# Kernel optimization log

Measured on AMD Instinct MI355X. Metric: run time of the kernel, lower is better.

## Reference

```python
import jax, jax.numpy as jnp
import numpy as np

N = 50000
E = 600000
DIN = 128
HID = 128
NG = 64


def _gat(x, src, dst, W, a_s, a_d, b, heads, dout, concat):
    # PyG GATConv (eval mode): per-head linear, edge attention logits,
    # segment softmax over destination nodes, weighted scatter-sum.
    n = x.shape[0]
    xp = (x @ W.T).reshape(n, heads, dout)                     # [n, H, D]
    e = jax.nn.leaky_relu(jnp.sum(xp * a_s, -1)[src] + jnp.sum(xp * a_d, -1)[dst], 0.2)  # [Etot, H]
    m = jax.ops.segment_max(e, dst, num_segments=n)
    ex = jnp.exp(e - m[dst])
    alpha = ex / jax.ops.segment_sum(ex, dst, num_segments=n)[dst]
    out = jax.ops.segment_sum(xp[src] * alpha[:, :, None], dst, num_segments=n)  # [n, H, D]
    out = out.reshape(n, heads * dout) if concat else out.mean(axis=1)
    return out + b


def _forward(x, edge_index, batch, Wi1, bi1, Wi2, bi2, Wg0, As0, Ad0, bg0, Wg1, As1, Ad1, bg1, Wg2, As2, Ad2, bg2, Wg3, As3, Ad3, bg3, We1, be1, We2, be2, Wc1, bc1, Wc2, bc2, Wc3, bc3):
    n = x.shape[0]
    loops = jnp.arange(n, dtype=edge_index.dtype)              # add_self_loops=True
    src = jnp.concatenate([edge_index[0], loops])
    dst = jnp.concatenate([edge_index[1], loops])
    # input_proj (dropout is a no-op in eval)
    h = jax.nn.relu(x @ Wi1.T + bi1) @ Wi2.T + bi2
    specs = [(Wg0, As0, Ad0, bg0, 8, 16, True),
             (Wg1, As1, Ad1, bg1, 8, 16, True),
             (Wg2, As2, Ad2, bg2, 8, 16, True),
             (Wg3, As3, Ad3, bg3, 1, 128, False)]
    for i, (W, a_s, a_d, b, hd, do, cc) in enumerate(specs):
        res = h
        h = jax.nn.elu(_gat(h, src, dst, W, a_s, a_d, b, hd, do, cc))
        if i > 0:
            h = h + res  # residual (dims always equal: 128)
    enh = h + (jax.nn.relu(h @ We1.T + be1) @ We2.T + be2)
    # per-graph mean / max / std (unbiased, ddof=1) pooling via segment reduces
    cnt = jax.ops.segment_sum(jnp.ones((n,), enh.dtype), batch, num_segments=NG)
    s = jax.ops.segment_sum(enh, batch, num_segments=NG)
    ss = jax.ops.segment_sum(enh * enh, batch, num_segments=NG)
    c = jnp.maximum(cnt, 1.0)[:, None]
    mean = s / c
    mx = jax.ops.segment_max(enh, batch, num_segments=NG)
    var = (ss - c * mean * mean) / jnp.maximum(cnt - 1.0, 1.0)[:, None]
    std = jnp.where(cnt[:, None] > 1.0, jnp.sqrt(jnp.maximum(var, 0.0)), 0.0)
    g = jnp.concatenate([mean, mx, std], axis=1)               # [NG, 3*HID]
    h1 = jax.nn.relu(g @ Wc1.T + bc1)
    h2 = jax.nn.relu(h1 @ Wc2.T + bc2)
    return h2 @ Wc3.T + bc3


def setup_inputs():
    ks = jax.random.split(jax.random.key(0), 32)

    def gl(k, o, i):
        return jax.random.normal(k, (o, i), jnp.float32) * jnp.sqrt(2.0 / (o + i))

    inp = {}
    inp["x"] = jax.random.normal(ks[0], (N, DIN), jnp.float32)
    inp["edge_index"] = jax.random.randint(ks[1], (2, E), 0, N, dtype=jnp.int32)
    inp["batch"] = jnp.sort(jax.random.randint(ks[2], (N,), 0, NG, dtype=jnp.int32))
    inp["Wi1"] = gl(ks[3], HID, DIN); inp["bi1"] = jnp.zeros((HID,), jnp.float32)
    inp["Wi2"] = gl(ks[4], HID, HID); inp["bi2"] = jnp.zeros((HID,), jnp.float32)
    for li in range(3):
        inp[f"Wg{li}"] = gl(ks[5 + li], HID, HID)
        inp[f"As{li}"] = jax.random.normal(ks[8 + li], (8, 16), jnp.float32) * 0.1
        inp[f"Ad{li}"] = jax.random.normal(ks[11 + li], (8, 16), jnp.float32) * 0.1
        inp[f"bg{li}"] = jnp.zeros((HID,), jnp.float32)
    inp["Wg3"] = gl(ks[14], HID, HID)
    inp["As3"] = jax.random.normal(ks[15], (1, HID), jnp.float32) * 0.1
    inp["Ad3"] = jax.random.normal(ks[16], (1, HID), jnp.float32) * 0.1
    inp["bg3"] = jnp.zeros((HID,), jnp.float32)
    inp["We1"] = gl(ks[17], HID, HID); inp["be1"] = jnp.zeros((HID,), jnp.float32)
    inp["We2"] = gl(ks[18], HID, HID); inp["be2"] = jnp.zeros((HID,), jnp.float32)
    inp["Wc1"] = gl(ks[19], HID, 3 * HID); inp["bc1"] = jnp.zeros((HID,), jnp.float32)
    inp["Wc2"] = gl(ks[20], HID // 2, HID); inp["bc2"] = jnp.zeros((HID // 2,), jnp.float32)
    inp["Wc3"] = gl(ks[21], 2, HID // 2); inp["bc3"] = jnp.zeros((2,), jnp.float32)
    return inp


def reference(x, edge_index, batch, Wi1, bi1, Wi2, bi2, Wg0, As0, Ad0, bg0, Wg1, As1, Ad1, bg1, Wg2, As2, Ad2, bg2, Wg3, As3, Ad3, bg3, We1, be1, We2, be2, Wc1, bc1, Wc2, bc2, Wc3, bc3):
    return _forward(x, edge_index, batch, Wi1, bi1, Wi2, bi2, Wg0, As0, Ad0, bg0, Wg1, As1, Ad1, bg1, Wg2, As2, Ad2, bg2, Wg3, As3, Ad3, bg3, We1, be1, We2, be2, Wc1, bc1, Wc2, bc2, Wc3, bc3)
```

## Files before the change

kernel.cpp:

```cpp
#include <hip/hip_runtime.h>
#include <hip/hip_fp16.h>
#include <cstddef>

typedef _Float16 f16;
typedef f16 f16x8 __attribute__((ext_vector_type(8)));
typedef float f32x4 __attribute__((ext_vector_type(4)));

__device__ __forceinline__ unsigned f2mono(float f){
  unsigned u = __float_as_uint(f);
  return (u & 0x80000000u) ? ~u : (u | 0x80000000u);
}
__device__ __forceinline__ float mono2f(unsigned u){
  return (u & 0x80000000u) ? __uint_as_float(u & 0x7fffffffu) : __uint_as_float(~u);
}

struct WPtrs { const float* w[8]; };
__global__ void k_wcast(WPtrs p, f16* __restrict__ Wh){
  int wi = blockIdx.y;
  const float* W = p.w[wi];
  f16* dst = Wh + (size_t)wi * 16384;
  int i = (blockIdx.x*256 + threadIdx.x) * 8;
  float4 v0 = *(const float4*)(W + i), v1 = *(const float4*)(W + i + 4);
  f16x8 h = {(f16)v0.x,(f16)v0.y,(f16)v0.z,(f16)v0.w,
             (f16)v1.x,(f16)v1.y,(f16)v1.z,(f16)v1.w};
  *(f16x8*)(dst + i) = h;
}

template<typename TIN, bool RES>
__global__ __launch_bounds__(256) void k_gemm2(
    const TIN* __restrict__ in, const f16* __restrict__ W1, const f16* __restrict__ W2,
    const float* __restrict__ b1, const float* __restrict__ b2,
    const float* __restrict__ res, float* __restrict__ outF, __half* __restrict__ outH, int n)
{
  constexpr int LDW = 130;
  __shared__ f16 Wl[128*LDW];
  __shared__ f16 Al[32*LDW];
  __shared__ f16 Ml[32*LDW];
  const int tid = threadIdx.x;
  const int r0 = blockIdx.x * 32;
#pragma unroll
  for (int i = 0; i < 8; i++){
    int u = tid + 256*i; int row = u >> 4, c8 = (u & 15) * 8;
    *(f16x8*)&Wl[row*LDW + c8] = *(const f16x8*)(W1 + (size_t)row*128 + c8);
  }
#pragma unroll
  for (int i = 0; i < 2; i++){
    int u = tid + 256*i; int row = u >> 4, c8 = (u & 15) * 8;
    int gr = r0 + row;
    f16x8 v = {};
    if (gr < n){
      if constexpr (__is_same(TIN, __half)){
        v = *(const f16x8*)((const f16*)in + (size_t)gr*128 + c8);
      } else {
        const float4* q = (const float4*)((const float*)in + (size_t)gr*128 + c8);
        float4 v0 = q[0], v1 = q[1];
        v = f16x8{(f16)v0.x,(f16)v0.y,(f16)v0.z,(f16)v0.w,
                  (f16)v1.x,(f16)v1.y,(f16)v1.z,(f16)v1.w};
      }
    }
    *(f16x8*)&Al[row*LDW + c8] = v;
  }
  __syncthreads();
  const int wv = tid >> 6, lane = tid & 63;
  const int l15 = lane & 15, quad = lane >> 4;
  f32x4 acc[2][2] = {};
  {
    const f16* Ab = &Al[l15*LDW + quad*8];
    const f16* Bb = &Wl[(wv*32 + l15)*LDW + quad*8];
#pragma unroll
    for (int kc = 0; kc < 4; kc++){
      f16x8 a0 = *(const f16x8*)(Ab + kc*32);
      f16x8 a1 = *(const f16x8*)(Ab + 16*LDW + kc*32);
#pragma unroll
      for (int nt = 0; nt < 2; nt++){
        f16x8 b = *(const f16x8*)(Bb + nt*16*LDW + kc*32);
        acc[0][nt] = __builtin_amdgcn_mfma_f32_16x16x32_f16(a0, b, acc[0][nt], 0, 0, 0);
        acc[1][nt] = __builtin_amdgcn_mfma_f32_16x16x32_f16(a1, b, acc[1][nt], 0, 0, 0);
      }
    }
  }
#pragma unroll
  for (int nt = 0; nt < 2; nt++){
    int col = wv*32 + nt*16 + l15;
    float bv = b1[col];
#pragma unroll
    for (int rh = 0; rh < 2; rh++)
#pragma unroll
      for (int reg = 0; reg < 4; reg++){
        int row = rh*16 + quad*4 + reg;
        Ml[row*LDW + col] = (f16)fmaxf(acc[rh][nt][reg] + bv, 0.f);
      }
  }
  __syncthreads();
#pragma unroll
  for (int i = 0; i < 8; i++){
    int u = tid + 256*i; int row = u >> 4, c8 = (u & 15) * 8;
    *(f16x8*)&Wl[row*LDW + c8] = *(const f16x8*)(W2 + (size_t)row*128 + c8);
  }
  __syncthreads();
  f32x4 acc2[2][2] = {};
  {
    const f16* Ab = &Ml[l15*LDW + quad*8];
    const f16* Bb = &Wl[(wv*32 + l15)*LDW + quad*8];
#pragma unroll
    for (int kc = 0; kc < 4; kc++){
      f16x8 a0 = *(const f16x8*)(Ab + kc*32);
      f16x8 a1 = *(const f16x8*)(Ab + 16*LDW + kc*32);
#pragma unroll
      for (int nt = 0; nt < 2; nt++){
        f16x8 b = *(const f16x8*)(Bb + nt*16*LDW + kc*32);
        acc2[0][nt] = __builtin_amdgcn_mfma_f32_16x16x32_f16(a0, b, acc2[0][nt], 0, 0, 0);
        acc2[1][nt] = __builtin_amdgcn_mfma_f32_16x16x32_f16(a1, b, acc2[1][nt], 0, 0, 0);
      }
    }
  }
#pragma unroll
  for (int nt = 0; nt < 2; nt++){
    int col = wv*32 + nt*16 + l15;
    float bv = b2[col];
#pragma unroll
    for (int rh = 0; rh < 2; rh++)
#pragma unroll
      for (int reg = 0; reg < 4; reg++){
        int gr = r0 + rh*16 + quad*4 + reg;
        if (gr >= n) continue;
        float o = acc2[rh][nt][reg] + bv;
        if constexpr (RES){
          o += res[(size_t)gr*128 + col];
          outF[(size_t)gr*128 + col] = o;
        } else {
          outH[(size_t)gr*128 + col] = __float2half(o);
        }
      }
  }
}

template<int PREP>
__global__ __launch_bounds__(256) void k_gat_gemm(
    const __half* __restrict__ in, const f16* __restrict__ Wm,
    const float* __restrict__ As, const float* __restrict__ Ad,
    float* __restrict__ es, float* __restrict__ ed,
    __half* __restrict__ outH, int n)
{
  constexpr int LDW = 130;
  __shared__ f16 Wl[64*LDW];
  __shared__ f16 Al[32*LDW];
  const int tid = threadIdx.x;
  const int ch = blockIdx.x & 1;
  const int r0 = (blockIdx.x >> 1) * 32;
#pragma unroll
  for (int i = 0; i < 4; i++){
    int u = tid + 256*i; int row = u >> 4, c8 = (u & 15) * 8;
    *(f16x8*)&Wl[row*LDW + c8] = *(const f16x8*)(Wm + (size_t)(ch*64 + row)*128 + c8);
  }
#pragma unroll
  for (int i = 0; i < 2; i++){
    int u = tid + 256*i; int row = u >> 4, c8 = (u & 15) * 8;
    int gr = r0 + row;
    f16x8 v = {};
    if (gr < n) v = *(const f16x8*)((const f16*)in + (size_t)gr*128 + c8);
    *(f16x8*)&Al[row*LDW + c8] = v;
  }
  __syncthreads();
  const int wv = tid >> 6, lane = tid & 63;
  const int l15 = lane & 15, quad = lane >> 4;
  const int rh = wv & 1, cq = wv >> 1;
  f32x4 acc[2] = {};
  const f16* Ab = &Al[(rh*16 + l15)*LDW + quad*8];
  const f16* Bb = &Wl[(cq*32 + l15)*LDW + quad*8];
#pragma unroll
  for (int kc = 0; kc < 4; kc++){
    f16x8 a = *(const f16x8*)(Ab + kc*32);
#pragma unroll
    for (int nt = 0; nt < 2; nt++){
      f16x8 b = *(const f16x8*)(Bb + nt*16*LDW + kc*32);
      acc[nt] = __builtin_amdgcn_mfma_f32_16x16x32_f16(a, b, acc[nt], 0, 0, 0);
    }
  }
#pragma unroll
  for (int nt = 0; nt < 2; nt++){
    int col = ch*64 + cq*32 + nt*16 + l15;
#pragma unroll
    for (int reg = 0; reg < 4; reg++){
      int gr = r0 + rh*16 + quad*4 + reg;
      if (gr < n) outH[(size_t)gr*128 + col] = __float2half(acc[nt][reg]);
    }
  }
  if constexpr (PREP == 1){
#pragma unroll
    for (int nt = 0; nt < 2; nt++){
      int hh = ch*4 + cq*2 + nt;
      float as_ = As[hh*16 + l15], ad_ = Ad[hh*16 + l15];
#pragma unroll
      for (int reg = 0; reg < 4; reg++){
        float se = acc[nt][reg] * as_;
        float sd = acc[nt][reg] * ad_;
#pragma unroll
        for (int off = 1; off < 16; off <<= 1){
          se += __shfl_xor(se, off); sd += __shfl_xor(sd, off);
        }
        int gr = r0 + rh*16 + quad*4 + reg;
        if (l15 == 0 && gr < n){ es[gr*8 + hh] = se; ed[gr*8 + hh] = sd; }
      }
    }
  } else {
    float as_[2], ad_[2];
#pragma unroll
    for (int nt = 0; nt < 2; nt++){
      int col = ch*64 + cq*32 + nt*16 + l15;
      as_[nt] = As[col]; ad_[nt] = Ad[col];
    }
#pragma unroll
    for (int reg = 0; reg < 4; reg++){
      float se = acc[0][reg]*as_[0] + acc[1][reg]*as_[1];
      float sd = acc[0][reg]*ad_[0] + acc[1][reg]*ad_[1];
#pragma unroll
      for (int off = 1; off < 16; off <<= 1){
        se += __shfl_xor(se, off); sd += __shfl_xor(sd, off);
      }
      int gr = r0 + rh*16 + quad*4 + reg;
      if (l15 == 0 && gr < n){ atomicAdd(&es[gr], se); atomicAdd(&ed[gr], sd); }
    }
  }
}

__global__ void k_deg(const int* __restrict__ ei, int* __restrict__ deg, int E, int N){
  int t = blockIdx.x*blockDim.x + threadIdx.x;
  if (t >= E + N) return;
  int d = (t < E) ? ei[E + t] : (t - E);
  atomicAdd(&deg[d], 1);
}
__global__ void k_scan1(const int* __restrict__ deg, int* __restrict__ bsum, int N){
  __shared__ int sd[256];
  int i = blockIdx.x*256 + threadIdx.x;
  sd[threadIdx.x] = (i < N) ? deg[i] : 0;
  __syncthreads();
  for (int s = 128; s > 0; s >>= 1){
    if (threadIdx.x < s) sd[threadIdx.x] += sd[threadIdx.x + s];
    __syncthreads();
  }
  if (threadIdx.x == 0) bsum[blockIdx.x] = sd[0];
}
__global__ void k_scan2(const int* __restrict__ bsum, int* __restrict__ boff, int nb){
  __shared__ int sd[256];
  int t = threadIdx.x;
  int v = (t < nb) ? bsum[t] : 0;
  sd[t] = v;
  __syncthreads();
  for (int s = 1; s < 256; s <<= 1){
    int u = (t >= s) ? sd[t - s] : 0;
    __syncthreads();
    sd[t] += u;
    __syncthreads();
  }
  if (t < nb) boff[t] = sd[t] - v;
}
__global__ void k_scan3(const int* __restrict__ deg, const int* __restrict__ boff,
                        int* __restrict__ rowptr, int N){
  __shared__ int sd[256];
  int tid = threadIdx.x;
  int i = blockIdx.x*256 + tid;
  sd[tid] = (i < N) ? deg[i] : 0;
  __syncthreads();
  for (int s = 1; s < 256; s <<= 1){
    int t = (tid >= s) ? sd[tid - s] : 0;
    __syncthreads();
    sd[tid] += t;
    __syncthreads();
  }
  if (i < N) rowptr[i+1] = boff[blockIdx.x] + sd[tid];
  if (i == 0) rowptr[0] = 0;
}
__global__ void k_fill(const int* __restrict__ ei, const int* __restrict__ rowptr,
                       int* __restrict__ fil, int* __restrict__ csr, int E, int N){
  int t = blockIdx.x*blockDim.x + threadIdx.x;
  if (t >= E + N) return;
  int s, d;
  if (t < E){ s = ei[t]; d = ei[E + t]; } else { s = d = t - E; }
  int pos = rowptr[d] + atomicAdd(&fil[d], 1);
  csr[pos] = s;
}

template<int H, int D>
__global__ __launch_bounds__(256) void k_aggregate(
    const __half* __restrict__ xp, const float* __restrict__ es, const float* __restrict__ ed,
    const int* __restrict__ rowptr, const int* __restrict__ csr,
    const float* __restrict__ bg, const float* res,
    float* out, __half* __restrict__ outH, int N)
{
  int gw = (blockIdx.x*256 + threadIdx.x) >> 6;
  if (gw >= N) return;
  const int lane = threadIdx.x & 63;
  const int j0 = lane*2;
  const int h0 = (H == 8) ? (lane >> 3) : 0;
  const int k8 = lane & 7;
  int beg = rowptr[gw], end = rowptr[gw+1];
  float edv = ed[gw*H + h0];
  float den = 0.f, a0 = 0.f, a1 = 0.f;
  for (int t = beg; t < end; t += 8){
    int nb = end - t; if (nb > 8) nb = 8;
    int idx = t + (k8 < nb ? k8 : nb - 1);
    int sE = csr[idx];
    float e = es[sE*H + h0] + edv;
    e = e > 0.f ? e : 0.2f*e;
    if (k8 >= nb) e = -1e30f;
    float w = __expf(e);
#pragma unroll
    for (int k = 0; k < 8; k++){
      float wk = __shfl(w, (h0 << 3) + k);
      int   sk = __shfl(sE, k);
      float2 f = __half22float2(*(const __half2*)(xp + (size_t)sk*128 + j0));
      den += wk; a0 += wk*f.x; a1 += wk*f.y;
    }
  }
  float inv = 1.f / den;
  float o0 = a0*inv + bg[j0];
  float o1 = a1*inv + bg[j0+1];
  o0 = o0 > 0.f ? o0 : __expf(o0) - 1.f;
  o1 = o1 > 0.f ? o1 : __expf(o1) - 1.f;
  if (res){ o0 += res[(size_t)gw*128 + j0]; o1 += res[(size_t)gw*128 + j0 + 1]; }
  *(float2*)(out + (size_t)gw*128 + j0) = make_float2(o0, o1);
  *(__half2*)(outH + (size_t)gw*128 + j0) = __floats2half2_rn(o0, o1);
}

__global__ __launch_bounds__(128) void k_pool(const float* __restrict__ enh,
    const int* __restrict__ batch, float* __restrict__ Ps, float* __restrict__ Pss,
    unsigned* __restrict__ Pmx, float* __restrict__ Pcnt, int N)
{
  int tid = threadIdx.x;
  int n0 = blockIdx.x * 128;
  if (n0 >= N) return;
  int n1 = min(n0 + 128, N);
  int cur = batch[n0];
  float sum = 0.f, ssq = 0.f, mx = -1e30f, cnt = 0.f;
  auto flush = [&](int b){
    atomicAdd(&Ps[b*128 + tid], sum);
    atomicAdd(&Pss[b*128 + tid], ssq);
    atomicMax(&Pmx[b*128 + tid], f2mono(mx));
    if (tid == 0) atomicAdd(&Pcnt[b], cnt);
  };
  for (int i = n0; i < n1; i++){
    int b = batch[i];
    if (b != cur){ flush(cur); cur = b; sum = 0.f; ssq = 0.f; mx = -1e30f; cnt = 0.f; }
    float v = enh[(size_t)i*128 + tid];
    sum += v; ssq += v*v; mx = fmaxf(mx, v); cnt += 1.f;
  }
  flush(cur);
}

__global__ void k_poolcls(const float* __restrict__ Ps, const float* __restrict__ Pss,
    const unsigned* __restrict__ Pmx, const float* __restrict__ Pcnt,
    const float* __restrict__ Wc1, const float* __restrict__ bc1,
    const float* __restrict__ Wc2, const float* __restrict__ bc2,
    const float* __restrict__ Wc3, const float* __restrict__ bc3,
    float* __restrict__ out)
{
  __shared__ float gs[384];
  __shared__ float hs[128];
  __shared__ float h2[64];
  int b = blockIdx.x, j = threadIdx.x;
  float cnt = Pcnt[b];
  float c = fmaxf(cnt, 1.f);
  float mean = Ps[b*128 + j] / c;
  float var = (Pss[b*128 + j] - c*mean*mean) / fmaxf(cnt - 1.f, 1.f);
  float sd = (cnt > 1.f) ? sqrtf(fmaxf(var, 0.f)) : 0.f;
  gs[j] = mean; gs[128 + j] = mono2f(Pmx[b*128 + j]); gs[256 + j] = sd;
  __syncthreads();
  float acc = bc1[j];
  const float4* wr = (const float4*)(Wc1 + (size_t)j*384);
  for (int i = 0; i < 96; i++){
    float4 w = wr[i];
    acc += gs[i*4]*w.x + gs[i*4+1]*w.y + gs[i*4+2]*w.z + gs[i*4+3]*w.w;
  }
  hs[j] = fmaxf(acc, 0.f);
  __syncthreads();
  if (j < 64){
    float a2 = bc2[j];
    const float4* w2 = (const float4*)(Wc2 + (size_t)j*128);
    for (int i = 0; i < 32; i++){
      float4 w = w2[i];
      a2 += hs[i*4]*w.x + hs[i*4+1]*w.y + hs[i*4+2]*w.z + hs[i*4+3]*w.w;
    }
    h2[j] = fmaxf(a2, 0.f);
  }
  __syncthreads();
  if (j < 2){
    float a = bc3[j];
    for (int i = 0; i < 64; i++) a += h2[i] * Wc3[j*64 + i];
    out[b*2 + j] = a;
  }
}

extern "C" void kernel_launch(void* const* d_in, const int* in_sizes, int n_in,
                              void* d_out, int out_size, void* d_ws, size_t ws_size,
                              hipStream_t stream)
{
  const float* x    = (const float*)d_in[0];
  const int*  ei    = (const int*)d_in[1];
  const int*  batch = (const int*)d_in[2];
  const float* Wi1  = (const float*)d_in[3];  const float* bi1 = (const float*)d_in[4];
  const float* Wi2  = (const float*)d_in[5];  const float* bi2 = (const float*)d_in[6];
  const float* Wg[4]= {(const float*)d_in[7],(const float*)d_in[11],(const float*)d_in[15],(const float*)d_in[19]};
  const float* As[4]= {(const float*)d_in[8],(const float*)d_in[12],(const float*)d_in[16],(const float*)d_in[20]};
  const float* Ad[4]= {(const float*)d_in[9],(const float*)d_in[13],(const float*)d_in[17],(const float*)d_in[21]};
  const float* bg[4]= {(const float*)d_in[10],(const float*)d_in[14],(const float*)d_in[18],(const float*)d_in[22]};
  const float* We1  = (const float*)d_in[23]; const float* be1 = (const float*)d_in[24];
  const float* We2  = (const float*)d_in[25]; const float* be2 = (const float*)d_in[26];
  const float* Wc1  = (const float*)d_in[27]; const float* bc1 = (const float*)d_in[28];
  const float* Wc2  = (const float*)d_in[29]; const float* bc2 = (const float*)d_in[30];
  const float* Wc3  = (const float*)d_in[31]; const float* bc3 = (const float*)d_in[32];
  float* outp = (float*)d_out;

  const int N = in_sizes[2];
  const int E = in_sizes[1] / 2;
  const int Etot = E + N;

  float* base = (float*)d_ws;
  size_t off = 0;
  auto alloc = [&](size_t elems) -> float* {
    float* p = base + off;
    off += (elems + 3) & ~(size_t)3;
    return p;
  };
  float* A    = alloc((size_t)N * 128);
  __half* Xh  = (__half*)alloc((size_t)N * 64);
  __half* Ah  = (__half*)alloc((size_t)N * 64);
  f16* Wh     = (f16*)alloc(8 * 8192);
  float* es   = alloc((size_t)N * 8);
  float* ed   = alloc((size_t)N * 8);
  float* Ps   = alloc(64 * 128);
  float* Pss  = alloc(64 * 128);
  unsigned* Pmx = (unsigned*)alloc(64 * 128);
  float* Pcnt = alloc(64);
  int* deg    = (int*)alloc(N);
  int* fil    = (int*)alloc(N);
  float* es3  = alloc(N);
  float* ed3  = alloc(N);
  size_t zend = off;
  int* rowptr = (int*)alloc(N + 1);
  int* bsum   = (int*)alloc(512);
  int* boff   = (int*)alloc(512);
  int* csr    = (int*)alloc(Etot);
  (void)ws_size; (void)n_in; (void)out_size;

  (void)hipMemsetAsync(Ps, 0, (size_t)((base + zend) - Ps) * sizeof(float), stream);

  WPtrs wp;
  wp.w[0]=Wi1; wp.w[1]=Wi2; wp.w[2]=Wg[0]; wp.w[3]=Wg[1]; wp.w[4]=Wg[2]; wp.w[5]=Wg[3]; wp.w[6]=We1; wp.w[7]=We2;
  k_wcast<<<dim3(8, 8), 256, 0, stream>>>(wp, Wh);

  const int g2 = (N + 31) / 32;
  const int gtiles = 2 * g2;
  k_gemm2<float, false><<<g2, 256, 0, stream>>>(x, Wh + 0*16384, Wh + 1*16384, bi1, bi2,
                                                nullptr, nullptr, Ah, N);

  const int nb = (N + 255) / 256;
  k_deg  <<<(Etot + 255) / 256, 256, 0, stream>>>(ei, deg, E, N);
  k_scan1<<<nb, 256, 0, stream>>>(deg, bsum, N);
  k_scan2<<<1, 256, 0, stream>>>(bsum, boff, nb);
  k_scan3<<<nb, 256, 0, stream>>>(deg, boff, rowptr, N);
  k_fill <<<(Etot + 255) / 256, 256, 0, stream>>>(ei, rowptr, fil, csr, E, N);

  for (int l = 0; l < 4; l++){
    if (l < 3){
      k_gat_gemm<1><<<gtiles, 256, 0, stream>>>(Ah, Wh + (size_t)(2+l)*16384, As[l], Ad[l],
                                                es, ed, Xh, N);
      k_aggregate<8,16><<<(N + 3) / 4, 256, 0, stream>>>(Xh, es, ed, rowptr, csr, bg[l],
                                                         l > 0 ? A : nullptr, A, Ah, N);
    } else {
      k_gat_gemm<2><<<gtiles, 256, 0, stream>>>(Ah, Wh + 5*16384, As[3], Ad[3],
                                                es3, ed3, Xh, N);
      k_aggregate<1,128><<<(N + 3) / 4, 256, 0, stream>>>(Xh, es3, ed3, rowptr, csr, bg[3],
                                                          A, A, Ah, N);
    }
  }

  k_gemm2<__half, true><<<g2, 256, 0, stream>>>(Ah, Wh + 6*16384, Wh + 7*16384, be1, be2,
                                                A, A, nullptr, N);

  k_pool   <<<(N + 127) / 128, 128, 0, stream>>>(A, batch, Ps, Pss, Pmx, Pcnt, N);
  k_poolcls<<<64, 128, 0, stream>>>(Ps, Pss, Pmx, Pcnt, Wc1, bc1, Wc2, bc2, Wc3, bc3, outp);
}
```

Baseline: 585.3 us.

## Stage GEMM epilogues through LDS, prefetch aggregate indices, shrink pool chunks

The k_gemm2 and k_gat_gemm epilogues now stage MFMA results in shared memory, so each row is written to global memory with wide coalesced vector stores instead of scattered scalar stores. k_aggregate prefetches the next batch of CSR indices and source logits one iteration ahead and issues all eight neighbor feature loads before accumulating, to expose more memory-level parallelism. k_pool uses 32-node chunks instead of 128 to launch more blocks. The cost is extra LDS traffic, additional barriers, more registers in aggregate, and more atomics in pooling.

```diff
diff --git a/kernel.cpp b/kernel.cpp
--- a/kernel.cpp
+++ b/kernel.cpp
@@ -114,6 +114,8 @@
       }
     }
   }
+  __syncthreads();
+  float* Cf = (float*)Wl;
 #pragma unroll
   for (int nt = 0; nt < 2; nt++){
     int col = wv*32 + nt*16 + l15;
@@ -122,16 +124,38 @@
     for (int rh = 0; rh < 2; rh++)
 #pragma unroll
       for (int reg = 0; reg < 4; reg++){
-        int gr = r0 + rh*16 + quad*4 + reg;
-        if (gr >= n) continue;
-        float o = acc2[rh][nt][reg] + bv;
-        if constexpr (RES){
-          o += res[(size_t)gr*128 + col];
-          outF[(size_t)gr*128 + col] = o;
-        } else {
-          outH[(size_t)gr*128 + col] = __float2half(o);
-        }
-      }
+        int row = rh*16 + quad*4 + reg;
+        Cf[row*132 + col] = acc2[rh][nt][reg] + bv;
+      }
+  }
+  __syncthreads();
+  if constexpr (RES){
+#pragma unroll
+    for (int i = 0; i < 4; i++){
+      int u = tid + 256*i;
+      int row = u >> 5, c4 = (u & 31) * 4;
+      int gr = r0 + row;
+      if (gr < n){
+        float4 r4 = *(const float4*)(res + (size_t)gr*128 + c4);
+        float4 v = *(float4*)&Cf[row*132 + c4];
+        v.x += r4.x; v.y += r4.y; v.z += r4.z; v.w += r4.w;
+        *(float4*)(outF + (size_t)gr*128 + c4) = v;
+      }
+    }
+  } else {
+#pragma unroll
+    for (int i = 0; i < 2; i++){
+      int u = tid + 256*i;
+      int row = u >> 4, c8 = (u & 15) * 8;
+      int gr = r0 + row;
+      if (gr < n){
+        float4 a = *(float4*)&Cf[row*132 + c8];
+        float4 b = *(float4*)&Cf[row*132 + c8 + 4];
+        f16x8 h = {(f16)a.x,(f16)a.y,(f16)a.z,(f16)a.w,
+                   (f16)b.x,(f16)b.y,(f16)b.z,(f16)b.w};
+        *(f16x8*)((f16*)outH + (size_t)gr*128 + c8) = h;
+      }
+    }
   }
 }
 
@@ -177,15 +201,6 @@
       acc[nt] = __builtin_amdgcn_mfma_f32_16x16x32_f16(a, b, acc[nt], 0, 0, 0);
     }
   }
-#pragma unroll
-  for (int nt = 0; nt < 2; nt++){
-    int col = ch*64 + cq*32 + nt*16 + l15;
-#pragma unroll
-    for (int reg = 0; reg < 4; reg++){
-      int gr = r0 + rh*16 + quad*4 + reg;
-      if (gr < n) outH[(size_t)gr*128 + col] = __float2half(acc[nt][reg]);
-    }
-  }
   if constexpr (PREP == 1){
 #pragma unroll
     for (int nt = 0; nt < 2; nt++){
@@ -221,6 +236,24 @@
       int gr = r0 + rh*16 + quad*4 + reg;
       if (l15 == 0 && gr < n){ atomicAdd(&es[gr], se); atomicAdd(&ed[gr], sd); }
     }
+  }
+  __syncthreads();
+  f16* St = Al;
+#pragma unroll
+  for (int nt = 0; nt < 2; nt++){
+    int c2 = cq*32 + nt*16 + l15;
+#pragma unroll
+    for (int reg = 0; reg < 4; reg++){
+      int row = rh*16 + quad*4 + reg;
+      St[row*72 + c2] = (f16)acc[nt][reg];
+    }
+  }
+  __syncthreads();
+  {
+    int row = tid >> 3, c8 = (tid & 7) * 8;
+    int gr = r0 + row;
+    if (gr < n)
+      *(f16x8*)((f16*)outH + (size_t)gr*128 + ch*64 + c8) = *(f16x8*)&St[row*72 + c8];
   }
 }
 
@@ -297,20 +330,35 @@
   int beg = rowptr[gw], end = rowptr[gw+1];
   float edv = ed[gw*H + h0];
   float den = 0.f, a0 = 0.f, a1 = 0.f;
+  int idx = beg + k8; if (idx >= end) idx = end - 1;
+  int sE = csr[idx];
+  float ev = es[sE*H + h0];
   for (int t = beg; t < end; t += 8){
     int nb = end - t; if (nb > 8) nb = 8;
-    int idx = t + (k8 < nb ? k8 : nb - 1);
-    int sE = csr[idx];
-    float e = es[sE*H + h0] + edv;
+    int sE_c = sE; float ev_c = ev;
+    int tn = t + 8;
+    if (tn < end){
+      int idxn = tn + k8; if (idxn >= end) idxn = end - 1;
+      sE = csr[idxn];
+      ev = es[sE*H + h0];
+    }
+    float e = ev_c + edv;
     e = e > 0.f ? e : 0.2f*e;
     if (k8 >= nb) e = -1e30f;
     float w = __expf(e);
+    float wk[8]; int sk[8];
 #pragma unroll
     for (int k = 0; k < 8; k++){
-      float wk = __shfl(w, (h0 << 3) + k);
-      int   sk = __shfl(sE, k);
-      float2 f = __half22float2(*(const __half2*)(xp + (size_t)sk*128 + j0));
-      den += wk; a0 += wk*f.x; a1 += wk*f.y;
+      wk[k] = __shfl(w, (h0 << 3) + k);
+      sk[k] = __shfl(sE_c, k);
+    }
+    float2 f[8];
+#pragma unroll
+    for (int k = 0; k < 8; k++)
+      f[k] = __half22float2(*(const __half2*)(xp + (size_t)sk[k]*128 + j0));
+#pragma unroll
+    for (int k = 0; k < 8; k++){
+      den += wk[k]; a0 += wk[k]*f[k].x; a1 += wk[k]*f[k].y;
     }
   }
   float inv = 1.f / den;
@@ -328,9 +376,9 @@
     unsigned* __restrict__ Pmx, float* __restrict__ Pcnt, int N)
 {
   int tid = threadIdx.x;
-  int n0 = blockIdx.x * 128;
+  int n0 = blockIdx.x * 32;
   if (n0 >= N) return;
-  int n1 = min(n0 + 128, N);
+  int n1 = min(n0 + 32, N);
   int cur = batch[n0];
   float sum = 0.f, ssq = 0.f, mx = -1e30f, cnt = 0.f;
   auto flush = [&](int b){
@@ -478,6 +526,6 @@
   k_gemm2<__half, true><<<g2, 256, 0, stream>>>(Ah, Wh + 6*16384, Wh + 7*16384, be1, be2,
                                                 A, A, nullptr, N);
 
-  k_pool   <<<(N + 127) / 128, 128, 0, stream>>>(A, batch, Ps, Pss, Pmx, Pcnt, N);
+  k_pool   <<<(N + 31) / 32, 128, 0, stream>>>(A, batch, Ps, Pss, Pmx, Pcnt, N);
   k_poolcls<<<64, 128, 0, stream>>>(Ps, Pss, Pmx, Pcnt, Wc1, bc1, Wc2, bc2, Wc3, bc3, outp);
 }
```

Result: faster. 567.9 us (-3.0%).
